# Performance work log

Measured on AMD Instinct MI355X. Metric: run time of the kernel, lower is better.

The kernel has to match this reference:

```python
import jax, jax.numpy as jnp
import numpy as np

B, S, D = 32, 1024, 256
F_, K = 256, 3
T = 8192
LN_EPS = 1e-5


def _conv1d(x, w, b, padding):
    # x: [B, S, C_in], w: [C_out, C_in, K] -> [B, S, C_out]
    y = jax.lax.conv_general_dilated(
        x.transpose(0, 2, 1), w, window_strides=(1,),
        padding=[(padding, padding)], dimension_numbers=('NCH', 'OIH', 'NCH'))
    return y.transpose(0, 2, 1) + b


def _layernorm(x, g, b):
    mu = jnp.mean(x, axis=-1, keepdims=True)
    var = jnp.mean(jnp.square(x - mu), axis=-1, keepdims=True)
    return (x - mu) * jax.lax.rsqrt(var + LN_EPS) * g + b


def setup_inputs() -> dict:
    key = jax.random.key(0)
    ks = jax.random.split(key, 8)
    sc = 0.02
    return {
        'x': jax.random.normal(ks[0], (B, S, D), dtype=jnp.float32),
        'mask': jnp.zeros((B, S), dtype=bool),
        'duration': jax.random.randint(ks[1], (B, S), 0, 8, dtype=jnp.int32),
        'max_len': T,
        'conv1_w': jax.random.normal(ks[2], (F_, D, K), dtype=jnp.float32) * sc,
        'conv1_b': jnp.zeros((F_,), dtype=jnp.float32),
        'ln1_g': jnp.ones((F_,), dtype=jnp.float32),
        'ln1_b': jnp.zeros((F_,), dtype=jnp.float32),
        'conv2_w': jax.random.normal(ks[3], (F_, F_, K), dtype=jnp.float32) * sc,
        'conv2_b': jnp.zeros((F_,), dtype=jnp.float32),
        'ln2_g': jnp.ones((F_,), dtype=jnp.float32),
        'ln2_b': jnp.zeros((F_,), dtype=jnp.float32),
        'lin_w': jax.random.normal(ks[4], (F_, 1), dtype=jnp.float32) * sc,
        'lin_b': jnp.zeros((1,), dtype=jnp.float32),
    }


def reference(x, mask, duration, max_len, conv1_w, conv1_b, ln1_g, ln1_b,
              conv2_w, conv2_b, ln2_g, ln2_b, lin_w, lin_b):
    # ---- duration predictor (eval mode: dropout = identity) ----
    h = _conv1d(x, conv1_w, conv1_b, (K - 1) // 2)
    h = _layernorm(jax.nn.relu(h), ln1_g, ln1_b)
    h = _conv1d(h, conv2_w, conv2_b, 1)
    h = _layernorm(jax.nn.relu(h), ln2_g, ln2_b)
    log_dur = (h @ lin_w + lin_b)[..., 0]  # [B, S]
    log_dur = jnp.where(mask, 0.0, log_dur)

    # ---- length regulator: repeat_interleave + pad, done as one gather ----
    dur = duration.astype(jnp.int32)
    cum = jnp.cumsum(dur, axis=1)                                   # [B, S]
    t = jnp.arange(max_len, dtype=jnp.int32)                        # [T]
    src_idx = jax.vmap(lambda c: jnp.searchsorted(c, t, side='right'))(cum)  # [B, T]
    mel_len = jnp.minimum(cum[:, -1], max_len)                      # [B]
    valid = t[None, :] < mel_len[:, None]                           # [B, T]
    src_idx = jnp.clip(src_idx, 0, x.shape[1] - 1)
    out = jnp.take_along_axis(x, src_idx[:, :, None], axis=1)       # [B, T, D]
    out = jnp.where(valid[:, :, None], out, 0.0)
    # duration_target path -> duration_rounded = duration, mel_mask stays None
    return out, log_dur, dur, mel_len
```

## Files before the change

kernel.cpp:

```cpp
#include <hip/hip_runtime.h>
#include <cstddef>

constexpr int Bb   = 32;
constexpr int Ss   = 1024;
constexpr int Dd   = 256;
constexpr int Ff   = 256;
constexpr int TMAX = 8192;
constexpr int MM   = Bb * Ss;
constexpr int KK   = 768;
constexpr int SP   = 1026;
constexpr float LN_EPS = 1e-5f;
constexpr int PIT  = 72;

typedef __bf16 bf16x8 __attribute__((ext_vector_type(8)));
typedef __bf16 bf16x4 __attribute__((ext_vector_type(4)));
typedef float  f32x4  __attribute__((ext_vector_type(4)));

__global__ __launch_bounds__(256) void pack_w_k(
    const float* __restrict__ w1, const float* __restrict__ w2,
    __bf16* __restrict__ wTT1, __bf16* __restrict__ wTT2)
{
    int i = blockIdx.x * 256 + threadIdx.x;
    const float* w = w1;
    __bf16* o = wTT1;
    int j = i;
    if (j >= Ff * KK) { j -= Ff * KK; w = w2; o = wTT2; }
    int d  = j & 255;
    int fk = j >> 8;
    int f  = fk / 3;
    int k  = fk - f * 3;
    o[(size_t)f * KK + k * 256 + d] = (__bf16)w[((size_t)(f * 256 + d)) * 3 + k];
}

constexpr int NMAIN = Bb * SP * 64;
constexpr int NPAD  = Bb * 2 * 64;

__global__ __launch_bounds__(256) void pack_x_k(
    const float* __restrict__ x, __bf16* __restrict__ xp1,
    __bf16* __restrict__ xp2)
{
    int i = blockIdx.x * 256 + threadIdx.x;
    if (i >= NMAIN) {
        int j = i - NMAIN;
        if (j < NPAD) {
            int b = j >> 7;
            int r = (j >> 6) & 1;
            int d = (j & 63) * 4;
            *(bf16x4*)&xp2[((size_t)b * SP + (size_t)r * (SP - 1)) * 256 + d] =
                (bf16x4)(__bf16)0.f;
        }
        return;
    }
    int e4  = i * 4;
    int row = e4 >> 8;
    int d   = e4 & 255;
    int b   = row / SP;
    int j   = row - b * SP;
    bf16x4 o;
    if (j == 0 || j == SP - 1) {
        o = (bf16x4)(__bf16)0.f;
    } else {
        float4 v = *(const float4*)&x[(((size_t)(b << 10) + (j - 1)) << 8) + d];
        o[0] = (__bf16)v.x; o[1] = (__bf16)v.y;
        o[2] = (__bf16)v.z; o[3] = (__bf16)v.w;
    }
    *(bf16x4*)&xp1[((size_t)row << 8) + d] = o;
}

template<int MODE>
__global__ __launch_bounds__(256, 3) void gemm_fused(
    const __bf16* __restrict__ Ap,
    const __bf16* __restrict__ Bw,
    const float* __restrict__ bias,
    const float* __restrict__ g, const float* __restrict__ bt,
    const float* __restrict__ lw, const float* __restrict__ lb,
    const unsigned char* __restrict__ mask,
    __bf16* __restrict__ outB, float* __restrict__ outF)
{
    __shared__ __bf16 As[64 * PIT];
    __shared__ __bf16 Bs[256 * PIT];

    const int tid  = threadIdx.x;
    const int m0   = blockIdx.x * 64;
    const int bb   = m0 >> 10;
    const int s0   = m0 & 1023;
    const int wave = tid >> 6;
    const int lane = tid & 63;
    const int wn   = wave * 64;
    const int lm   = lane & 15;
    const int lk   = lane >> 4;

    f32x4 acc[4][4] = {};

    for (int step = 0; step < KK / 64; ++step) {
        const int kk0  = step * 64;
        const int kblk = kk0 >> 8;
        const int d0   = kk0 & 255;
        const __bf16* aSrc = Ap + (((size_t)(bb * SP + s0 + kblk)) << 8) + d0;
        #pragma unroll
        for (int i = 0; i < 2; ++i) {
            int c = i * 256 + tid, r = c >> 3, q = c & 7;
            *(bf16x8*)&As[r * PIT + q * 8] =
                *(const bf16x8*)&aSrc[((size_t)r << 8) + q * 8];
        }
        const __bf16* bSrc = Bw + kk0;
        #pragma unroll
        for (int i = 0; i < 8; ++i) {
            int c = i * 256 + tid, r = c >> 3, q = c & 7;
            *(bf16x8*)&Bs[r * PIT + q * 8] =
                *(const bf16x8*)&bSrc[(size_t)r * KK + q * 8];
        }
        __syncthreads();
        #pragma unroll
        for (int kc = 0; kc < 2; ++kc) {
            bf16x8 af[4], bfr[4];
            #pragma unroll
            for (int mi = 0; mi < 4; ++mi)
                af[mi] = *(const bf16x8*)&As[(mi * 16 + lm) * PIT + kc * 32 + lk * 8];
            #pragma unroll
            for (int ni = 0; ni < 4; ++ni)
                bfr[ni] = *(const bf16x8*)&Bs[(wn + ni * 16 + lm) * PIT + kc * 32 + lk * 8];
            #pragma unroll
            for (int mi = 0; mi < 4; ++mi)
                #pragma unroll
                for (int ni = 0; ni < 4; ++ni)
                    acc[mi][ni] = __builtin_amdgcn_mfma_f32_16x16x32_bf16(
                        af[mi], bfr[ni], acc[mi][ni], 0, 0, 0);
        }
        __syncthreads();
    }

    float* scrS = (float*)As;
    float* scrQ = scrS + 256;

    float s_[4][4] = {}, q_[4][4] = {};
    #pragma unroll
    for (int ni = 0; ni < 4; ++ni) {
        float bv = bias[wn + ni * 16 + lm];
        #pragma unroll
        for (int mi = 0; mi < 4; ++mi)
            #pragma unroll
            for (int r = 0; r < 4; ++r) {
                float h = fmaxf(acc[mi][ni][r] + bv, 0.f);
                acc[mi][ni][r] = h;
                s_[mi][r] += h;
                q_[mi][r] += h * h;
            }
    }
    #pragma unroll
    for (int off = 1; off < 16; off <<= 1)
        #pragma unroll
        for (int mi = 0; mi < 4; ++mi)
            #pragma unroll
            for (int r = 0; r < 4; ++r) {
                s_[mi][r] += __shfl_xor(s_[mi][r], off, 64);
                q_[mi][r] += __shfl_xor(q_[mi][r], off, 64);
            }
    if (lm == 0) {
        #pragma unroll
        for (int mi = 0; mi < 4; ++mi)
            #pragma unroll
            for (int r = 0; r < 4; ++r) {
                int row = mi * 16 + lk * 4 + r;
                scrS[wave * 64 + row] = s_[mi][r];
                scrQ[wave * 64 + row] = q_[mi][r];
            }
    }
    __syncthreads();

    float mu[4][4], rs[4][4];
    #pragma unroll
    for (int mi = 0; mi < 4; ++mi)
        #pragma unroll
        for (int r = 0; r < 4; ++r) {
            int row = mi * 16 + lk * 4 + r;
            float S = scrS[row] + scrS[64 + row] + scrS[128 + row] + scrS[192 + row];
            float Q = scrQ[row] + scrQ[64 + row] + scrQ[128 + row] + scrQ[192 + row];
            float m_ = S * (1.f / 256.f);
            float v_ = Q * (1.f / 256.f) - m_ * m_;
            mu[mi][r] = m_;
            rs[mi][r] = rsqrtf(v_ + LN_EPS);
        }

    if constexpr (MODE == 0) {
        size_t obase = ((size_t)(bb * SP + s0 + 1)) << 8;
        #pragma unroll
        for (int ni = 0; ni < 4; ++ni) {
            int col = wn + ni * 16 + lm;
            float gv = g[col], bv2 = bt[col];
            #pragma unroll
            for (int mi = 0; mi < 4; ++mi)
                #pragma unroll
                for (int r = 0; r < 4; ++r) {
                    int row = mi * 16 + lk * 4 + r;
                    float o = (acc[mi][ni][r] - mu[mi][r]) * rs[mi][r] * gv + bv2;
                    outB[obase + ((size_t)row << 8) + col] = (__bf16)o;
                }
        }
    } else {
        float p_[4][4] = {};
        #pragma unroll
        for (int ni = 0; ni < 4; ++ni) {
            int col = wn + ni * 16 + lm;
            float gv = g[col], bv2 = bt[col], wv = lw[col];
            #pragma unroll
            for (int mi = 0; mi < 4; ++mi)
                #pragma unroll
                for (int r = 0; r < 4; ++r) {
                    float o = (acc[mi][ni][r] - mu[mi][r]) * rs[mi][r] * gv + bv2;
                    p_[mi][r] += o * wv;
                }
        }
        #pragma unroll
        for (int off = 1; off < 16; off <<= 1)
            #pragma unroll
            for (int mi = 0; mi < 4; ++mi)
                #pragma unroll
                for (int r = 0; r < 4; ++r)
                    p_[mi][r] += __shfl_xor(p_[mi][r], off, 64);
        __syncthreads();
        if (lm == 0) {
            #pragma unroll
            for (int mi = 0; mi < 4; ++mi)
                #pragma unroll
                for (int r = 0; r < 4; ++r)
                    scrS[wave * 64 + (mi * 16 + lk * 4 + r)] = p_[mi][r];
        }
        __syncthreads();
        if (tid < 64) {
            int row = tid;
            float v = scrS[row] + scrS[64 + row] + scrS[128 + row] + scrS[192 + row]
                      + lb[0];
            if (mask[m0 + row]) v = 0.f;
            outF[m0 + row] = v;
        }
    }
}

__global__ __launch_bounds__(256) void cumsum_ss_k(
    const int* __restrict__ dur, float* __restrict__ dur_out,
    float* __restrict__ mel_out, int* __restrict__ idx)
{
    int b = blockIdx.x, tid = threadIdx.x;
    __shared__ int ic[1024];
    __shared__ int sc[256];
    int4 d4 = ((const int4*)(dur + b * 1024))[tid];
    int l0 = d4.x, l1 = l0 + d4.y, l2 = l1 + d4.z, l3 = l2 + d4.w;
    sc[tid] = l3;
    __syncthreads();
    for (int off = 1; off < 256; off <<= 1) {
        int v = (tid >= off) ? sc[tid - off] : 0;
        __syncthreads();
        sc[tid] += v;
        __syncthreads();
    }
    int excl = sc[tid] - l3;
    ((int4*)ic)[tid] = make_int4(excl + l0, excl + l1, excl + l2, excl + l3);
    ((float4*)(dur_out + b * 1024))[tid] =
        make_float4((float)d4.x, (float)d4.y, (float)d4.z, (float)d4.w);
    if (tid == 255) mel_out[b] = (float)min(excl + l3, TMAX);
    __syncthreads();
    int mel = min(ic[1023], TMAX);
    for (int t = tid; t < TMAX; t += 256) {
        int lo = 0, hi = 1024;
        #pragma unroll
        for (int it = 0; it < 10; ++it) {
            int mid = (lo + hi) >> 1;
            if (ic[mid] <= t) lo = mid + 1; else hi = mid;
        }
        idx[b * TMAX + t] = (t < mel) ? min(lo, 1023) : -1;
    }
}

__global__ __launch_bounds__(256) void gather_k(
    const float4* __restrict__ xv, const int* __restrict__ idx,
    float4* __restrict__ outv)
{
    int g   = blockIdx.x * 256 + threadIdx.x;
    int row = g >> 6;
    int col = g & 63;
    int s = idx[row];
    float4 v = make_float4(0.f, 0.f, 0.f, 0.f);
    if (s >= 0) {
        int b = row >> 13;
        v = xv[((size_t)(b << 10) + s) * 64 + col];
    }
    outv[g] = v;
}

extern "C" void kernel_launch(void* const* d_in, const int* in_sizes, int n_in,
                              void* d_out, int out_size, void* d_ws, size_t ws_size,
                              hipStream_t stream)
{
    const float* x            = (const float*)d_in[0];
    const unsigned char* mask = (const unsigned char*)d_in[1];
    const int* duration       = (const int*)d_in[2];
    const float* w1  = (const float*)d_in[4];
    const float* b1  = (const float*)d_in[5];
    const float* g1  = (const float*)d_in[6];
    const float* be1 = (const float*)d_in[7];
    const float* w2  = (const float*)d_in[8];
    const float* b2  = (const float*)d_in[9];
    const float* g2  = (const float*)d_in[10];
    const float* be2 = (const float*)d_in[11];
    const float* lw  = (const float*)d_in[12];
    const float* lb  = (const float*)d_in[13];

    float* out        = (float*)d_out;
    float* out0       = out;
    float* out_logdur = out + (size_t)Bb * TMAX * Dd;
    float* out_dur    = out_logdur + (size_t)Bb * Ss;
    float* out_mel    = out_dur + (size_t)Bb * Ss;

    char* ws = (char*)d_ws;
    __bf16* xp1  = (__bf16*)ws;
    __bf16* xp2  = xp1 + (size_t)Bb * SP * 256;
    __bf16* wTT1 = xp2 + (size_t)Bb * SP * 256;
    __bf16* wTT2 = wTT1 + (size_t)Ff * KK;
    int*    idx  = (int*)(wTT2 + (size_t)Ff * KK);

    pack_w_k   <<<2 * Ff * KK / 256, 256, 0, stream>>>(w1, w2, wTT1, wTT2);
    pack_x_k   <<<(NMAIN + NPAD) / 256, 256, 0, stream>>>(x, xp1, xp2);
    gemm_fused<0><<<MM / 64, 256, 0, stream>>>(
        xp1, wTT1, b1, g1, be1, nullptr, nullptr, nullptr, xp2, nullptr);
    gemm_fused<1><<<MM / 64, 256, 0, stream>>>(
        xp2, wTT2, b2, g2, be2, lw, lb, mask, nullptr, out_logdur);
    cumsum_ss_k<<<Bb, 256, 0, stream>>>(duration, out_dur, out_mel, idx);
    gather_k   <<<(Bb * TMAX * Dd / 4) / 256, 256, 0, stream>>>(
                   (const float4*)x, idx, (float4*)out0);
}
```

Measured before the change: 380.9 us.

## Fuse prep kernels, read fp32 x directly in conv1 GEMM, enlarge M tile

Merges weight packing, xp2 pad zeroing and the duration cumsum/searchsorted into one prep kernel, and drops the separate x-to-bf16 padded pack. The first conv GEMM now loads fp32 x directly, converts to bf16 while staging into shared memory, and handles the padding with a bounds check. Both GEMMs move to 128-row tiles with 512 threads (8 waves as 2x4), which halves how often each block reloads the weight tile. The cost is occupancy capped at one block per CU and fp32 A loads that move twice the bytes of the old bf16 path.

Result: no change. 384.0 us (+0.8%).

```diff
diff --git a/kernel.cpp b/kernel.cpp
--- a/kernel.cpp
+++ b/kernel.cpp
@@ -16,234 +16,41 @@
 typedef __bf16 bf16x4 __attribute__((ext_vector_type(4)));
 typedef float  f32x4  __attribute__((ext_vector_type(4)));
 
-__global__ __launch_bounds__(256) void pack_w_k(
+__global__ __launch_bounds__(256) void prep_k(
     const float* __restrict__ w1, const float* __restrict__ w2,
-    __bf16* __restrict__ wTT1, __bf16* __restrict__ wTT2)
-{
-    int i = blockIdx.x * 256 + threadIdx.x;
-    const float* w = w1;
-    __bf16* o = wTT1;
-    int j = i;
-    if (j >= Ff * KK) { j -= Ff * KK; w = w2; o = wTT2; }
-    int d  = j & 255;
-    int fk = j >> 8;
-    int f  = fk / 3;
-    int k  = fk - f * 3;
-    o[(size_t)f * KK + k * 256 + d] = (__bf16)w[((size_t)(f * 256 + d)) * 3 + k];
-}
-
-constexpr int NMAIN = Bb * SP * 64;
-constexpr int NPAD  = Bb * 2 * 64;
-
-__global__ __launch_bounds__(256) void pack_x_k(
-    const float* __restrict__ x, __bf16* __restrict__ xp1,
+    __bf16* __restrict__ wTT1, __bf16* __restrict__ wTT2,
+    const int* __restrict__ dur, float* __restrict__ dur_out,
+    float* __restrict__ mel_out, int* __restrict__ idx,
     __bf16* __restrict__ xp2)
 {
-    int i = blockIdx.x * 256 + threadIdx.x;
-    if (i >= NMAIN) {
-        int j = i - NMAIN;
-        if (j < NPAD) {
-            int b = j >> 7;
-            int r = (j >> 6) & 1;
-            int d = (j & 63) * 4;
-            *(bf16x4*)&xp2[((size_t)b * SP + (size_t)r * (SP - 1)) * 256 + d] =
-                (bf16x4)(__bf16)0.f;
-        }
-        return;
-    }
-    int e4  = i * 4;
-    int row = e4 >> 8;
-    int d   = e4 & 255;
-    int b   = row / SP;
-    int j   = row - b * SP;
-    bf16x4 o;
-    if (j == 0 || j == SP - 1) {
-        o = (bf16x4)(__bf16)0.f;
-    } else {
-        float4 v = *(const float4*)&x[(((size_t)(b << 10) + (j - 1)) << 8) + d];
-        o[0] = (__bf16)v.x; o[1] = (__bf16)v.y;
-        o[2] = (__bf16)v.z; o[3] = (__bf16)v.w;
-    }
-    *(bf16x4*)&xp1[((size_t)row << 8) + d] = o;
-}
-
-template<int MODE>
-__global__ __launch_bounds__(256, 3) void gemm_fused(
-    const __bf16* __restrict__ Ap,
-    const __bf16* __restrict__ Bw,
-    const float* __restrict__ bias,
-    const float* __restrict__ g, const float* __restrict__ bt,
-    const float* __restrict__ lw, const float* __restrict__ lb,
-    const unsigned char* __restrict__ mask,
-    __bf16* __restrict__ outB, float* __restrict__ outF)
-{
-    __shared__ __bf16 As[64 * PIT];
-    __shared__ __bf16 Bs[256 * PIT];
-
-    const int tid  = threadIdx.x;
-    const int m0   = blockIdx.x * 64;
-    const int bb   = m0 >> 10;
-    const int s0   = m0 & 1023;
-    const int wave = tid >> 6;
-    const int lane = tid & 63;
-    const int wn   = wave * 64;
-    const int lm   = lane & 15;
-    const int lk   = lane >> 4;
-
-    f32x4 acc[4][4] = {};
-
-    for (int step = 0; step < KK / 64; ++step) {
-        const int kk0  = step * 64;
-        const int kblk = kk0 >> 8;
-        const int d0   = kk0 & 255;
-        const __bf16* aSrc = Ap + (((size_t)(bb * SP + s0 + kblk)) << 8) + d0;
-        #pragma unroll
-        for (int i = 0; i < 2; ++i) {
-            int c = i * 256 + tid, r = c >> 3, q = c & 7;
-            *(bf16x8*)&As[r * PIT + q * 8] =
-                *(const bf16x8*)&aSrc[((size_t)r << 8) + q * 8];
-        }
-        const __bf16* bSrc = Bw + kk0;
-        #pragma unroll
-        for (int i = 0; i < 8; ++i) {
-            int c = i * 256 + tid, r = c >> 3, q = c & 7;
-            *(bf16x8*)&Bs[r * PIT + q * 8] =
-                *(const bf16x8*)&bSrc[(size_t)r * KK + q * 8];
-        }
-        __syncthreads();
-        #pragma unroll
-        for (int kc = 0; kc < 2; ++kc) {
-            bf16x8 af[4], bfr[4];
-            #pragma unroll
-            for (int mi = 0; mi < 4; ++mi)
-                af[mi] = *(const bf16x8*)&As[(mi * 16 + lm) * PIT + kc * 32 + lk * 8];
-            #pragma unroll
-            for (int ni = 0; ni < 4; ++ni)
-                bfr[ni] = *(const bf16x8*)&Bs[(wn + ni * 16 + lm) * PIT + kc * 32 + lk * 8];
-            #pragma unroll
-            for (int mi = 0; mi < 4; ++mi)
-                #pragma unroll
-                for (int ni = 0; ni < 4; ++ni)
-                    acc[mi][ni] = __builtin_amdgcn_mfma_f32_16x16x32_bf16(
-                        af[mi], bfr[ni], acc[mi][ni], 0, 0, 0);
-        }
-        __syncthreads();
-    }
-
-    float* scrS = (float*)As;
-    float* scrQ = scrS + 256;
-
-    float s_[4][4] = {}, q_[4][4] = {};
-    #pragma unroll
-    for (int ni = 0; ni < 4; ++ni) {
-        float bv = bias[wn + ni * 16 + lm];
-        #pragma unroll
-        for (int mi = 0; mi < 4; ++mi)
-            #pragma unroll
-            for (int r = 0; r < 4; ++r) {
-                float h = fmaxf(acc[mi][ni][r] + bv, 0.f);
-                acc[mi][ni][r] = h;
-                s_[mi][r] += h;
-                q_[mi][r] += h * h;
-            }
-    }
-    #pragma unroll
-    for (int off = 1; off < 16; off <<= 1)
-        #pragma unroll
-        for (int mi = 0; mi < 4; ++mi)
-            #pragma unroll
-            for (int r = 0; r < 4; ++r) {
-                s_[mi][r] += __shfl_xor(s_[mi][r], off, 64);
-                q_[mi][r] += __shfl_xor(q_[mi][r], off, 64);
-            }
-    if (lm == 0) {
-        #pragma unroll
-        for (int mi = 0; mi < 4; ++mi)
-            #pragma unroll
-            for (int r = 0; r < 4; ++r) {
-                int row = mi * 16 + lk * 4 + r;
-                scrS[wave * 64 + row] = s_[mi][r];
-                scrQ[wave * 64 + row] = q_[mi][r];
-            }
-    }
-    __syncthreads();
-
-    float mu[4][4], rs[4][4];
-    #pragma unroll
-    for (int mi = 0; mi < 4; ++mi)
-        #pragma unroll
-        for (int r = 0; r < 4; ++r) {
-            int row = mi * 16 + lk * 4 + r;
-            float S = scrS[row] + scrS[64 + row] + scrS[128 + row] + scrS[192 + row];
-            float Q = scrQ[row] + scrQ[64 + row] + scrQ[128 + row] + scrQ[192 + row];
-            float m_ = S * (1.f / 256.f);
-            float v_ = Q * (1.f / 256.f) - m_ * m_;
-            mu[mi][r] = m_;
-            rs[mi][r] = rsqrtf(v_ + LN_EPS);
-        }
-
-    if constexpr (MODE == 0) {
-        size_t obase = ((size_t)(bb * SP + s0 + 1)) << 8;
-        #pragma unroll
-        for (int ni = 0; ni < 4; ++ni) {
-            int col = wn + ni * 16 + lm;
-            float gv = g[col], bv2 = bt[col];
-            #pragma unroll
-            for (int mi = 0; mi < 4; ++mi)
-                #pragma unroll
-                for (int r = 0; r < 4; ++r) {
-                    int row = mi * 16 + lk * 4 + r;
-                    float o = (acc[mi][ni][r] - mu[mi][r]) * rs[mi][r] * gv + bv2;
-                    outB[obase + ((size_t)row << 8) + col] = (__bf16)o;
-                }
-        }
-    } else {
-        float p_[4][4] = {};
-        #pragma unroll
-        for (int ni = 0; ni < 4; ++ni) {
-            int col = wn + ni * 16 + lm;
-            float gv = g[col], bv2 = bt[col], wv = lw[col];
-            #pragma unroll
-            for (int mi = 0; mi < 4; ++mi)
-                #pragma unroll
-                for (int r = 0; r < 4; ++r) {
-                    float o = (acc[mi][ni][r] - mu[mi][r]) * rs[mi][r] * gv + bv2;
-                    p_[mi][r] += o * wv;
-                }
-        }
-        #pragma unroll
-        for (int off = 1; off < 16; off <<= 1)
-            #pragma unroll
-            for (int mi = 0; mi < 4; ++mi)
-                #pragma unroll
-                for (int r = 0; r < 4; ++r)
-                    p_[mi][r] += __shfl_xor(p_[mi][r], off, 64);
-        __syncthreads();
-        if (lm == 0) {
-            #pragma unroll
-            for (int mi = 0; mi < 4; ++mi)
-                #pragma unroll
-                for (int r = 0; r < 4; ++r)
-                    scrS[wave * 64 + (mi * 16 + lk * 4 + r)] = p_[mi][r];
-        }
-        __syncthreads();
-        if (tid < 64) {
-            int row = tid;
-            float v = scrS[row] + scrS[64 + row] + scrS[128 + row] + scrS[192 + row]
-                      + lb[0];
-            if (mask[m0 + row]) v = 0.f;
-            outF[m0 + row] = v;
-        }
-    }
-}
-
-__global__ __launch_bounds__(256) void cumsum_ss_k(
-    const int* __restrict__ dur, float* __restrict__ dur_out,
-    float* __restrict__ mel_out, int* __restrict__ idx)
-{
-    int b = blockIdx.x, tid = threadIdx.x;
     __shared__ int ic[1024];
     __shared__ int sc[256];
+    const int blk = blockIdx.x;
+    const int tid = threadIdx.x;
+
+    if (blk < 1536) {
+        int i = blk * 256 + tid;
+        const float* w = w1;
+        __bf16* o = wTT1;
+        int j = i;
+        if (j >= Ff * KK) { j -= Ff * KK; w = w2; o = wTT2; }
+        int d  = j & 255;
+        int fk = j >> 8;
+        int f  = fk / 3;
+        int k  = fk - f * 3;
+        o[(size_t)f * KK + k * 256 + d] = (__bf16)w[((size_t)(f * 256 + d)) * 3 + k];
+        return;
+    }
+    if (blk >= 1568) {
+        int j = (blk - 1568) * 256 + tid;
+        int b = j >> 7;
+        int r = (j >> 6) & 1;
+        int d = (j & 63) * 4;
+        *(bf16x4*)&xp2[((size_t)b * SP + (size_t)r * (SP - 1)) * 256 + d] =
+            (bf16x4)(__bf16)0.f;
+        return;
+    }
+    int b = blk - 1536;
     int4 d4 = ((const int4*)(dur + b * 1024))[tid];
     int l0 = d4.x, l1 = l0 + d4.y, l2 = l1 + d4.z, l3 = l2 + d4.w;
     sc[tid] = l3;
@@ -269,6 +76,203 @@
             if (ic[mid] <= t) lo = mid + 1; else hi = mid;
         }
         idx[b * TMAX + t] = (t < mel) ? min(lo, 1023) : -1;
+    }
+}
+
+template<int MODE>
+__global__ __launch_bounds__(512, 1) void gemm_fused(
+    const float* __restrict__ Xf,
+    const __bf16* __restrict__ Ap,
+    const __bf16* __restrict__ Bw,
+    const float* __restrict__ bias,
+    const float* __restrict__ g, const float* __restrict__ bt,
+    const float* __restrict__ lw, const float* __restrict__ lb,
+    const unsigned char* __restrict__ mask,
+    __bf16* __restrict__ outB, float* __restrict__ outF)
+{
+    __shared__ __bf16 As[128 * PIT];
+    __shared__ __bf16 Bs[256 * PIT];
+
+    const int tid  = threadIdx.x;
+    const int m0   = blockIdx.x * 128;
+    const int bb   = m0 >> 10;
+    const int s0   = m0 & 1023;
+    const int wave = tid >> 6;
+    const int lane = tid & 63;
+    const int wm   = (wave & 1) * 64;
+    const int wn   = (wave >> 1) * 64;
+    const int lm   = lane & 15;
+    const int lk   = lane >> 4;
+
+    f32x4 acc[4][4] = {};
+
+    for (int step = 0; step < KK / 64; ++step) {
+        const int kk0  = step * 64;
+        const int kblk = kk0 >> 8;
+        const int d0   = kk0 & 255;
+
+        if constexpr (MODE == 0) {
+            #pragma unroll
+            for (int i = 0; i < 4; ++i) {
+                int c = i * 512 + tid;
+                int r = c >> 4, q = c & 15;
+                int sg = s0 + r + kblk - 1;
+                bf16x4 o = (bf16x4)(__bf16)0.f;
+                if ((unsigned)sg < 1024u) {
+                    float4 v = *(const float4*)&Xf[
+                        (((size_t)(bb << 10) + sg) << 8) + d0 + q * 4];
+                    o[0] = (__bf16)v.x; o[1] = (__bf16)v.y;
+                    o[2] = (__bf16)v.z; o[3] = (__bf16)v.w;
+                }
+                *(bf16x4*)&As[r * PIT + q * 4] = o;
+            }
+        } else {
+            const __bf16* aSrc = Ap + (((size_t)(bb * SP + s0 + kblk)) << 8) + d0;
+            #pragma unroll
+            for (int i = 0; i < 2; ++i) {
+                int c = i * 512 + tid;
+                int r = c >> 3, q = c & 7;
+                *(bf16x8*)&As[r * PIT + q * 8] =
+                    *(const bf16x8*)&aSrc[((size_t)r << 8) + q * 8];
+            }
+        }
+        const __bf16* bSrc = Bw + kk0;
+        #pragma unroll
+        for (int i = 0; i < 4; ++i) {
+            int c = i * 512 + tid;
+            int r = c >> 3, q = c & 7;
+            *(bf16x8*)&Bs[r * PIT + q * 8] =
+                *(const bf16x8*)&bSrc[(size_t)r * KK + q * 8];
+        }
+        __syncthreads();
+
+        #pragma unroll
+        for (int kc = 0; kc < 2; ++kc) {
+            bf16x8 af[4], bfr[4];
+            #pragma unroll
+            for (int mi = 0; mi < 4; ++mi)
+                af[mi] = *(const bf16x8*)&As[(wm + mi * 16 + lm) * PIT + kc * 32 + lk * 8];
+            #pragma unroll
+            for (int ni = 0; ni < 4; ++ni)
+                bfr[ni] = *(const bf16x8*)&Bs[(wn + ni * 16 + lm) * PIT + kc * 32 + lk * 8];
+            #pragma unroll
+            for (int mi = 0; mi < 4; ++mi)
+                #pragma unroll
+                for (int ni = 0; ni < 4; ++ni)
+                    acc[mi][ni] = __builtin_amdgcn_mfma_f32_16x16x32_bf16(
+                        af[mi], bfr[ni], acc[mi][ni], 0, 0, 0);
+        }
+        __syncthreads();
+    }
+
+    float* scrS = (float*)As;
+    float* scrQ = scrS + 512;
+
+    float s_[4][4] = {}, q_[4][4] = {};
+    #pragma unroll
+    for (int ni = 0; ni < 4; ++ni) {
+        float bv = bias[wn + ni * 16 + lm];
+        #pragma unroll
+        for (int mi = 0; mi < 4; ++mi)
+            #pragma unroll
+            for (int r = 0; r < 4; ++r) {
+                float h = fmaxf(acc[mi][ni][r] + bv, 0.f);
+                acc[mi][ni][r] = h;
+                s_[mi][r] += h;
+                q_[mi][r] += h * h;
+            }
+    }
+    #pragma unroll
+    for (int off = 1; off < 16; off <<= 1)
+        #pragma unroll
+        for (int mi = 0; mi < 4; ++mi)
+            #pragma unroll
+            for (int r = 0; r < 4; ++r) {
+                s_[mi][r] += __shfl_xor(s_[mi][r], off, 64);
+                q_[mi][r] += __shfl_xor(q_[mi][r], off, 64);
+            }
+    if (lm == 0) {
+        #pragma unroll
+        for (int mi = 0; mi < 4; ++mi)
+            #pragma unroll
+            for (int r = 0; r < 4; ++r) {
+                int rl = mi * 16 + lk * 4 + r;
+                scrS[wave * 64 + rl] = s_[mi][r];
+                scrQ[wave * 64 + rl] = q_[mi][r];
+            }
+    }
+    __syncthreads();
+
+    const int half = wave & 1;
+    float mu[4][4], rs[4][4];
+    #pragma unroll
+    for (int mi = 0; mi < 4; ++mi)
+        #pragma unroll
+        for (int r = 0; r < 4; ++r) {
+            int rl = mi * 16 + lk * 4 + r;
+            float S = scrS[(0 + half) * 64 + rl] + scrS[(2 + half) * 64 + rl]
+                    + scrS[(4 + half) * 64 + rl] + scrS[(6 + half) * 64 + rl];
+            float Q = scrQ[(0 + half) * 64 + rl] + scrQ[(2 + half) * 64 + rl]
+                    + scrQ[(4 + half) * 64 + rl] + scrQ[(6 + half) * 64 + rl];
+            float m_ = S * (1.f / 256.f);
+            float v_ = Q * (1.f / 256.f) - m_ * m_;
+            mu[mi][r] = m_;
+            rs[mi][r] = rsqrtf(v_ + LN_EPS);
+        }
+
+    if constexpr (MODE == 0) {
+        size_t obase = ((size_t)(bb * SP + s0 + 1 + wm)) << 8;
+        #pragma unroll
+        for (int ni = 0; ni < 4; ++ni) {
+            int col = wn + ni * 16 + lm;
+            float gv = g[col], bv2 = bt[col];
+            #pragma unroll
+            for (int mi = 0; mi < 4; ++mi)
+                #pragma unroll
+                for (int r = 0; r < 4; ++r) {
+                    int rl = mi * 16 + lk * 4 + r;
+                    float o = (acc[mi][ni][r] - mu[mi][r]) * rs[mi][r] * gv + bv2;
+                    outB[obase + ((size_t)rl << 8) + col] = (__bf16)o;
+                }
+        }
+    } else {
+        float p_[4][4] = {};
+        #pragma unroll
+        for (int ni = 0; ni < 4; ++ni) {
+            int col = wn + ni * 16 + lm;
+            float gv = g[col], bv2 = bt[col], wv = lw[col];
+            #pragma unroll
+            for (int mi = 0; mi < 4; ++mi)
+                #pragma unroll
+                for (int r = 0; r < 4; ++r) {
+                    float o = (acc[mi][ni][r] - mu[mi][r]) * rs[mi][r] * gv + bv2;
+                    p_[mi][r] += o * wv;
+                }
+        }
+        #pragma unroll
+        for (int off = 1; off < 16; off <<= 1)
+            #pragma unroll
+            for (int mi = 0; mi < 4; ++mi)
+                #pragma unroll
+                for (int r = 0; r < 4; ++r)
+                    p_[mi][r] += __shfl_xor(p_[mi][r], off, 64);
+        __syncthreads();
+        if (lm == 0) {
+            #pragma unroll
+            for (int mi = 0; mi < 4; ++mi)
+                #pragma unroll
+                for (int r = 0; r < 4; ++r)
+                    scrS[wave * 64 + (mi * 16 + lk * 4 + r)] = p_[mi][r];
+        }
+        __syncthreads();
+        if (tid < 128) {
+            int gr = tid;
+            int h = gr >> 6, rl = gr & 63;
+            float v = scrS[(0 + h) * 64 + rl] + scrS[(2 + h) * 64 + rl]
+                    + scrS[(4 + h) * 64 + rl] + scrS[(6 + h) * 64 + rl] + lb[0];
+            if (mask[m0 + gr]) v = 0.f;
+            outF[m0 + gr] = v;
+        }
     }
 }
 
@@ -313,19 +317,17 @@
     float* out_mel    = out_dur + (size_t)Bb * Ss;
 
     char* ws = (char*)d_ws;
-    __bf16* xp1  = (__bf16*)ws;
-    __bf16* xp2  = xp1 + (size_t)Bb * SP * 256;
+    __bf16* xp2  = (__bf16*)ws;
     __bf16* wTT1 = xp2 + (size_t)Bb * SP * 256;
     __bf16* wTT2 = wTT1 + (size_t)Ff * KK;
     int*    idx  = (int*)(wTT2 + (size_t)Ff * KK);
 
-    pack_w_k   <<<2 * Ff * KK / 256, 256, 0, stream>>>(w1, w2, wTT1, wTT2);
-    pack_x_k   <<<(NMAIN + NPAD) / 256, 256, 0, stream>>>(x, xp1, xp2);
-    gemm_fused<0><<<MM / 64, 256, 0, stream>>>(
-        xp1, wTT1, b1, g1, be1, nullptr, nullptr, nullptr, xp2, nullptr);
-    gemm_fused<1><<<MM / 64, 256, 0, stream>>>(
-        xp2, wTT2, b2, g2, be2, lw, lb, mask, nullptr, out_logdur);
-    cumsum_ss_k<<<Bb, 256, 0, stream>>>(duration, out_dur, out_mel, idx);
-    gather_k   <<<(Bb * TMAX * Dd / 4) / 256, 256, 0, stream>>>(
-                   (const float4*)x, idx, (float4*)out0);
+    prep_k<<<1584, 256, 0, stream>>>(w1, w2, wTT1, wTT2,
+                                     duration, out_dur, out_mel, idx, xp2);
+    gemm_fused<0><<<MM / 128, 512, 0, stream>>>(
+        x, nullptr, wTT1, b1, g1, be1, nullptr, nullptr, nullptr, xp2, nullptr);
+    gemm_fused<1><<<MM / 128, 512, 0, stream>>>(
+        nullptr, xp2, wTT2, b2, g2, be2, lw, lb, mask, nullptr, out_logdur);
+    gather_k<<<(Bb * TMAX * Dd / 4) / 256, 256, 0, stream>>>(
+        (const float4*)x, idx, (float4*)out0);
 }
```
